# Performance work log

Hardware: AMD Instinct MI355X
Metric: run time of the kernel (lower is better)

Reference implementation:

```python
import jax, jax.numpy as jnp
import numpy as np

EMB = 768
EPS = 1e-5

def setup_inputs() -> dict:
    key = jax.random.key(0)
    ks = jax.random.split(key, 7)
    B, S, D = 8, 2048, EMB
    s = 1.0 / np.sqrt(D)
    return {
        "h_": jax.random.normal(ks[0], (B, S, D), dtype=jnp.float32),
        "ln_gamma": jnp.ones((D,), jnp.float32),
        "ln_beta": jnp.zeros((D,), jnp.float32),
        "wq": jax.random.normal(ks[1], (D, D), jnp.float32) * s,
        "bq": jax.random.normal(ks[2], (D,), jnp.float32) * 0.01,
        "wk": jax.random.normal(ks[3], (D, D), jnp.float32) * s,
        "bk": jax.random.normal(ks[4], (D,), jnp.float32) * 0.01,
    }

def reference(h_, ln_gamma, ln_beta, wq, bq, wk, bk):
    # LayerNorm over last dim
    mu = jnp.mean(h_, axis=-1, keepdims=True)
    var = jnp.mean(jnp.square(h_ - mu), axis=-1, keepdims=True)
    hn = (h_ - mu) * jax.lax.rsqrt(var + EPS) * ln_gamma + ln_beta
    # Q/K projections (torch Linear: x @ W^T + b; here wq is [D_in, D_out])
    q = jnp.einsum('bsd,de->bse', hn, wq) + bq
    k = jnp.einsum('bsd,de->bse', hn, wk) + bk
    # scores: q @ k^T (no sqrt(d) scaling, matching original)
    w = jnp.einsum('bqd,bkd->bqk', q, k)
    return jax.nn.softmax(w, axis=-1)
```

## Files before the change

kernel.cpp:

```cpp
#include <hip/hip_runtime.h>
#include <stdint.h>

#define EMB   768
#define BATCH 8
#define SEQ   2048
#define ROWS  (BATCH*SEQ)
#define EPS   1e-5f

#define BM 128
#define BN 128
#define BK 32
#define BK2 64

typedef _Float16 half8 __attribute__((ext_vector_type(8)));
typedef _Float16 half4 __attribute__((ext_vector_type(4)));
typedef float    floatx4 __attribute__((ext_vector_type(4)));

__device__ __forceinline__ void g2l16(const void* g, void* l) {
    __builtin_amdgcn_global_load_lds(
        (const __attribute__((address_space(1))) unsigned int*)g,
        (__attribute__((address_space(3))) unsigned int*)l,
        16, 0, 0);
}

__global__ __launch_bounds__(256) void split_w_kernel(
    const float* __restrict__ wq, const float* __restrict__ wk,
    _Float16* __restrict__ wq_hi, _Float16* __restrict__ wq_lo,
    _Float16* __restrict__ wk_hi, _Float16* __restrict__ wk_lo)
{
    const float* src = (blockIdx.y == 0) ? wq : wk;
    _Float16* dh     = (blockIdx.y == 0) ? wq_hi : wk_hi;
    _Float16* dl     = (blockIdx.y == 0) ? wq_lo : wk_lo;
    int i4 = blockIdx.x * 256 + threadIdx.x;
    float4 v = ((const float4*)src)[i4];
    half4 vh, vl;
    float c[4] = {v.x, v.y, v.z, v.w};
#pragma unroll
    for (int t = 0; t < 4; t++) {
        _Float16 hi = (_Float16)c[t];
        vh[t] = hi;
        vl[t] = (_Float16)(c[t] - (float)hi);
    }
    ((half4*)dh)[i4] = vh;
    ((half4*)dl)[i4] = vl;
}

__global__ __launch_bounds__(256) void wtilde_kernel(
    const float* __restrict__ wk, const float* __restrict__ bq,
    float* __restrict__ wt)
{
    int row  = blockIdx.x * 4 + (threadIdx.x >> 6);
    int lane = threadIdx.x & 63;
    const float4* r4 = (const float4*)(wk + (size_t)row * EMB);
    const float4* b4 = (const float4*)bq;
    float s = 0.f;
#pragma unroll
    for (int j = 0; j < 3; j++) {
        float4 a = r4[lane + j * 64];
        float4 b = b4[lane + j * 64];
        s += a.x * b.x + a.y * b.y + a.z * b.z + a.w * b.w;
    }
#pragma unroll
    for (int sh = 1; sh < 64; sh <<= 1) s += __shfl_xor(s, sh, 64);
    if (lane == 0) wt[row] = s;
}

__global__ __launch_bounds__(256) void ln_kernel(
    const float* __restrict__ h,
    const float* __restrict__ gamma,
    const float* __restrict__ beta,
    const float* __restrict__ wt,
    _Float16* __restrict__ hn_hi,
    float* __restrict__ v_out)
{
    int row  = blockIdx.x * 4 + (threadIdx.x >> 6);
    int lane = threadIdx.x & 63;
    const float4* hr4 = (const float4*)(h + (size_t)row * EMB);
    float4 x[3];
    float s1 = 0.f, s2 = 0.f;
#pragma unroll
    for (int j = 0; j < 3; j++) {
        x[j] = hr4[lane + j * 64];
        s1 += x[j].x + x[j].y + x[j].z + x[j].w;
        s2 += x[j].x * x[j].x + x[j].y * x[j].y + x[j].z * x[j].z + x[j].w * x[j].w;
    }
#pragma unroll
    for (int s = 1; s < 64; s <<= 1) {
        s1 += __shfl_xor(s1, s, 64);
        s2 += __shfl_xor(s2, s, 64);
    }
    float mu  = s1 * (1.0f / EMB);
    float var = s2 * (1.0f / EMB) - mu * mu;
    float rs  = rsqrtf(var + EPS);
    _Float16* oh = hn_hi + (size_t)row * EMB;
    float vsum = 0.f;
#pragma unroll
    for (int j = 0; j < 3; j++) {
        int e4 = lane + j * 64;
        float4 g = ((const float4*)gamma)[e4];
        float4 b = ((const float4*)beta)[e4];
        float4 w = ((const float4*)wt)[e4];
        float v[4] = {
            (x[j].x - mu) * rs * g.x + b.x,
            (x[j].y - mu) * rs * g.y + b.y,
            (x[j].z - mu) * rs * g.z + b.z,
            (x[j].w - mu) * rs * g.w + b.w };
        vsum += v[0] * w.x + v[1] * w.y + v[2] * w.z + v[3] * w.w;
        half4 vh;
#pragma unroll
        for (int t = 0; t < 4; t++) vh[t] = (_Float16)v[t];
        *(half4*)(oh + e4 * 4) = vh;
    }
#pragma unroll
    for (int s = 1; s < 64; s <<= 1) vsum += __shfl_xor(vsum, s, 64);
    if (lane == 0) v_out[row] = vsum;
}

__global__ __launch_bounds__(256) void gt_kernel(
    const _Float16* __restrict__ wk_hi, const _Float16* __restrict__ wk_lo,
    const _Float16* __restrict__ wq_hi, const _Float16* __restrict__ wq_lo,
    _Float16* __restrict__ gt_hi, _Float16* __restrict__ gt_lo)
{
    __shared__ __attribute__((aligned(16))) _Float16 Ah_s[BM * BK];
    __shared__ __attribute__((aligned(16))) _Float16 Al_s[BM * BK];
    __shared__ __attribute__((aligned(16))) _Float16 Bh_s[BN * BK];
    __shared__ __attribute__((aligned(16))) _Float16 Bl_s[BN * BK];

    int rowbase = blockIdx.y * BM;
    int colbase = blockIdx.x * BN;
    int tid  = threadIdx.x;
    int lane = tid & 63, wave = tid >> 6;
    int wrow = (wave >> 1) * 64, wcol = (wave & 1) * 64;

    floatx4 acc[4][4];
#pragma unroll
    for (int i = 0; i < 4; i++)
#pragma unroll
        for (int j = 0; j < 4; j++) acc[i][j] = (floatx4){0.f, 0.f, 0.f, 0.f};

    size_t arow = (size_t)(rowbase + tid / 4) * EMB;
    size_t brow = (size_t)(colbase + tid / 4) * EMB;
    int    boff = (tid % 4) * 16;
    const char* gAh = (const char*)(wk_hi + arow) + boff;
    const char* gAl = (const char*)(wk_lo + arow) + boff;
    const char* gBh = (const char*)(wq_hi + brow) + boff;
    const char* gBl = (const char*)(wq_lo + brow) + boff;
    char* lAh = (char*)Ah_s + tid * 16;
    char* lAl = (char*)Al_s + tid * 16;
    char* lBh = (char*)Bh_s + tid * 16;
    char* lBl = (char*)Bl_s + tid * 16;
    const size_t half_stride = (size_t)64 * EMB * 2;

    for (int k0 = 0; k0 < EMB; k0 += BK) {
        __syncthreads();
        g2l16(gAh, lAh); g2l16(gAh + half_stride, lAh + 4096);
        g2l16(gAl, lAl); g2l16(gAl + half_stride, lAl + 4096);
        g2l16(gBh, lBh); g2l16(gBh + half_stride, lBh + 4096);
        g2l16(gBl, lBl); g2l16(gBl + half_stride, lBl + 4096);
        gAh += 64; gAl += 64; gBh += 64; gBl += 64;
        __syncthreads();

        half8 ah[4], al[4], bh[4], bl[4];
#pragma unroll
        for (int i = 0; i < 4; i++) {
            int off = (wrow + i * 16 + (lane & 15)) * 64 + (lane >> 4) * 16;
            ah[i] = *(const half8*)((const char*)Ah_s + off);
            al[i] = *(const half8*)((const char*)Al_s + off);
        }
#pragma unroll
        for (int j = 0; j < 4; j++) {
            int off = (wcol + j * 16 + (lane & 15)) * 64 + (lane >> 4) * 16;
            bh[j] = *(const half8*)((const char*)Bh_s + off);
            bl[j] = *(const half8*)((const char*)Bl_s + off);
        }
#pragma unroll
        for (int i = 0; i < 4; i++)
#pragma unroll
            for (int j = 0; j < 4; j++) {
                acc[i][j] = __builtin_amdgcn_mfma_f32_16x16x32_f16(ah[i], bh[j], acc[i][j], 0, 0, 0);
                acc[i][j] = __builtin_amdgcn_mfma_f32_16x16x32_f16(ah[i], bl[j], acc[i][j], 0, 0, 0);
                acc[i][j] = __builtin_amdgcn_mfma_f32_16x16x32_f16(al[i], bh[j], acc[i][j], 0, 0, 0);
            }
    }

#pragma unroll
    for (int j = 0; j < 4; j++) {
        int col = colbase + wcol + j * 16 + (lane & 15);
#pragma unroll
        for (int i = 0; i < 4; i++) {
#pragma unroll
            for (int r = 0; r < 4; r++) {
                int row = rowbase + wrow + i * 16 + (lane >> 4) * 4 + r;
                float v = acc[i][j][r];
                _Float16 hi = (_Float16)v;
                gt_hi[(size_t)row * EMB + col] = hi;
                gt_lo[(size_t)row * EMB + col] = (_Float16)(v - (float)hi);
            }
        }
    }
}

__global__ __launch_bounds__(256) void t_kernel(
    const _Float16* __restrict__ hn_hi,
    const _Float16* __restrict__ gt_hi, const _Float16* __restrict__ gt_lo,
    _Float16* __restrict__ t_hi)
{
    __shared__ __attribute__((aligned(16))) _Float16 Ah_s[BM * BK2];
    __shared__ __attribute__((aligned(16))) _Float16 Bh_s[BN * BK2];
    __shared__ __attribute__((aligned(16))) _Float16 Bl_s[BN * BK2];

    int rowbase = blockIdx.y * BM;
    int colbase = blockIdx.x * BN;
    int tid  = threadIdx.x;
    int lane = tid & 63, wave = tid >> 6;
    int wrow = (wave >> 1) * 64, wcol = (wave & 1) * 64;

    floatx4 acc[4][4];
#pragma unroll
    for (int i = 0; i < 4; i++)
#pragma unroll
        for (int j = 0; j < 4; j++) acc[i][j] = (floatx4){0.f, 0.f, 0.f, 0.f};

    size_t arow = (size_t)(rowbase + tid / 8) * EMB;
    size_t brow = (size_t)(colbase + tid / 8) * EMB;
    int    boff = (tid % 8) * 16;
    const char* gAh = (const char*)(hn_hi + arow) + boff;
    const char* gBh = (const char*)(gt_hi + brow) + boff;
    const char* gBl = (const char*)(gt_lo + brow) + boff;
    char* lAh = (char*)Ah_s + tid * 16;
    char* lBh = (char*)Bh_s + tid * 16;
    char* lBl = (char*)Bl_s + tid * 16;
    const size_t pstride = (size_t)32 * EMB * 2;

    for (int k0 = 0; k0 < EMB; k0 += BK2) {
        __syncthreads();
#pragma unroll
        for (int p = 0; p < 4; p++) {
            g2l16(gAh + p * pstride, lAh + p * 4096);
            g2l16(gBh + p * pstride, lBh + p * 4096);
            g2l16(gBl + p * pstride, lBl + p * 4096);
        }
        gAh += 128; gBh += 128; gBl += 128;
        __syncthreads();

#pragma unroll
        for (int ko = 0; ko < 2; ko++) {
            half8 ah[4], bh[4], bl[4];
#pragma unroll
            for (int i = 0; i < 4; i++) {
                int off = (wrow + i * 16 + (lane & 15)) * 128 + ko * 64 + (lane >> 4) * 16;
                ah[i] = *(const half8*)((const char*)Ah_s + off);
            }
#pragma unroll
            for (int j = 0; j < 4; j++) {
                int off = (wcol + j * 16 + (lane & 15)) * 128 + ko * 64 + (lane >> 4) * 16;
                bh[j] = *(const half8*)((const char*)Bh_s + off);
                bl[j] = *(const half8*)((const char*)Bl_s + off);
            }
#pragma unroll
            for (int i = 0; i < 4; i++)
#pragma unroll
                for (int j = 0; j < 4; j++) {
                    acc[i][j] = __builtin_amdgcn_mfma_f32_16x16x32_f16(ah[i], bh[j], acc[i][j], 0, 0, 0);
                    acc[i][j] = __builtin_amdgcn_mfma_f32_16x16x32_f16(ah[i], bl[j], acc[i][j], 0, 0, 0);
                }
        }
    }

#pragma unroll
    for (int j = 0; j < 4; j++) {
        int col = colbase + wcol + j * 16 + (lane & 15);
#pragma unroll
        for (int i = 0; i < 4; i++) {
#pragma unroll
            for (int r = 0; r < 4; r++) {
                int row = rowbase + wrow + i * 16 + (lane >> 4) * 4 + r;
                t_hi[(size_t)row * EMB + col] = (_Float16)acc[i][j][r];
            }
        }
    }
}

__global__ __launch_bounds__(256) void scores_kernel(
    const _Float16* __restrict__ t_hi,
    const _Float16* __restrict__ hn_hi,
    const float* __restrict__ v_in,
    float* __restrict__ out,
    float2* __restrict__ state)
{
    __shared__ __attribute__((aligned(16))) _Float16 Ah_s[BM * BK2];
    __shared__ __attribute__((aligned(16))) _Float16 Bh_s[BN * BK2];
    __shared__ float red[128][2];

    int b = blockIdx.z;
    size_t base = (size_t)b * SEQ * EMB;
    int rowbase = blockIdx.y * BM;
    int colbase = blockIdx.x * BN;
    int tid  = threadIdx.x;
    int lane = tid & 63, wave = tid >> 6;
    int wrow = (wave >> 1) * 64, wcol = (wave & 1) * 64;

    floatx4 acc[4][4];
#pragma unroll
    for (int i = 0; i < 4; i++)
#pragma unroll
        for (int j = 0; j < 4; j++) acc[i][j] = (floatx4){0.f, 0.f, 0.f, 0.f};

    size_t arow = base + (size_t)(rowbase + tid / 8) * EMB;
    size_t brow = base + (size_t)(colbase + tid / 8) * EMB;
    int    boff = (tid % 8) * 16;
    const char* gAh = (const char*)(t_hi + arow) + boff;
    const char* gBh = (const char*)(hn_hi + brow) + boff;
    char* lAh = (char*)Ah_s + tid * 16;
    char* lBh = (char*)Bh_s + tid * 16;
    const size_t pstride = (size_t)32 * EMB * 2;

    for (int k0 = 0; k0 < EMB; k0 += BK2) {
        __syncthreads();
#pragma unroll
        for (int p = 0; p < 4; p++) {
            g2l16(gAh + p * pstride, lAh + p * 4096);
            g2l16(gBh + p * pstride, lBh + p * 4096);
        }
        gAh += 128; gBh += 128;
        __syncthreads();

#pragma unroll
        for (int ko = 0; ko < 2; ko++) {
            half8 ah[4], bh[4];
#pragma unroll
            for (int i = 0; i < 4; i++) {
                int off = (wrow + i * 16 + (lane & 15)) * 128 + ko * 64 + (lane >> 4) * 16;
                ah[i] = *(const half8*)((const char*)Ah_s + off);
            }
#pragma unroll
            for (int j = 0; j < 4; j++) {
                int off = (wcol + j * 16 + (lane & 15)) * 128 + ko * 64 + (lane >> 4) * 16;
                bh[j] = *(const half8*)((const char*)Bh_s + off);
            }
#pragma unroll
            for (int i = 0; i < 4; i++)
#pragma unroll
                for (int j = 0; j < 4; j++)
                    acc[i][j] = __builtin_amdgcn_mfma_f32_16x16x32_f16(ah[i], bh[j], acc[i][j], 0, 0, 0);
        }
    }

    const float* vb = v_in + (size_t)b * SEQ + colbase;
#pragma unroll
    for (int j = 0; j < 4; j++) {
        float vv = vb[wcol + j * 16 + (lane & 15)];
#pragma unroll
        for (int i = 0; i < 4; i++)
#pragma unroll
            for (int r = 0; r < 4; r++) acc[i][j][r] += vv;
    }

    float m1[4][4];
#pragma unroll
    for (int i = 0; i < 4; i++)
#pragma unroll
        for (int r = 0; r < 4; r++) {
            float m = fmaxf(fmaxf(acc[i][0][r], acc[i][1][r]), fmaxf(acc[i][2][r], acc[i][3][r]));
#pragma unroll
            for (int s = 1; s < 16; s <<= 1) m = fmaxf(m, __shfl_xor(m, s, 64));
            m1[i][r] = m;
        }
    if ((lane & 15) == 0) {
#pragma unroll
        for (int i = 0; i < 4; i++)
#pragma unroll
            for (int r = 0; r < 4; r++)
                red[wrow + i * 16 + (lane >> 4) * 4 + r][wave & 1] = m1[i][r];
    }
    __syncthreads();
    float mrow[4][4];
#pragma unroll
    for (int i = 0; i < 4; i++)
#pragma unroll
        for (int r = 0; r < 4; r++) {
            int rr = wrow + i * 16 + (lane >> 4) * 4 + r;
            mrow[i][r] = fmaxf(red[rr][0], red[rr][1]);
        }
    __syncthreads();

    float ls[4][4];
#pragma unroll
    for (int i = 0; i < 4; i++)
#pragma unroll
        for (int r = 0; r < 4; r++) {
            float s = 0.f;
#pragma unroll
            for (int j = 0; j < 4; j++) {
                float e = __expf(acc[i][j][r] - mrow[i][r]);
                acc[i][j][r] = e;
                s += e;
            }
#pragma unroll
            for (int sh = 1; sh < 16; sh <<= 1) s += __shfl_xor(s, sh, 64);
            ls[i][r] = s;
        }
    if ((lane & 15) == 0) {
#pragma unroll
        for (int i = 0; i < 4; i++)
#pragma unroll
            for (int r = 0; r < 4; r++)
                red[wrow + i * 16 + (lane >> 4) * 4 + r][wave & 1] = ls[i][r];
    }
    __syncthreads();

    size_t outbase = (size_t)b * SEQ * SEQ;
#pragma unroll
    for (int i = 0; i < 4; i++)
#pragma unroll
        for (int j = 0; j < 4; j++)
#pragma unroll
            for (int r = 0; r < 4; r++) {
                int row = rowbase + wrow + i * 16 + (lane >> 4) * 4 + r;
                int col = colbase + wcol + j * 16 + (lane & 15);
                out[outbase + (size_t)row * SEQ + col] = acc[i][j][r];
            }

    if ((wave & 1) == 0 && (lane & 15) == 0) {
#pragma unroll
        for (int i = 0; i < 4; i++)
#pragma unroll
            for (int r = 0; r < 4; r++) {
                int rr = wrow + i * 16 + (lane >> 4) * 4 + r;
                float l = red[rr][0] + red[rr][1];
                state[((size_t)b * SEQ + rowbase + rr) * 16 + blockIdx.x] =
                    make_float2(mrow[i][r], l);
            }
    }
}

__global__ __launch_bounds__(256) void fixup_kernel(
    float* __restrict__ out,
    const float2* __restrict__ state)
{
    int row  = blockIdx.x * 4 + (threadIdx.x >> 6);
    int lane = threadIdx.x & 63;
    const float2* st = state + (size_t)row * 16;
    float m[16], l[16];
    float M = -INFINITY;
#pragma unroll
    for (int t = 0; t < 16; t++) { float2 v = st[t]; m[t] = v.x; l[t] = v.y; M = fmaxf(M, m[t]); }
    float L = 0.f;
#pragma unroll
    for (int t = 0; t < 16; t++) { m[t] = __expf(m[t] - M); L += l[t] * m[t]; }
    float inv = 1.0f / L;
    float4* o4 = (float4*)(out + (size_t)row * SEQ);
#pragma unroll
    for (int c0 = 0; c0 < 8; c0++) {
        int i4 = c0 * 64 + lane;
        float s = m[i4 >> 5] * inv;
        float4 v = o4[i4];
        v.x *= s; v.y *= s; v.z *= s; v.w *= s;
        o4[i4] = v;
    }
}

extern "C" void kernel_launch(void* const* d_in, const int* in_sizes, int n_in,
                              void* d_out, int out_size, void* d_ws, size_t ws_size,
                              hipStream_t stream)
{
    const float* h  = (const float*)d_in[0];
    const float* g  = (const float*)d_in[1];
    const float* be = (const float*)d_in[2];
    const float* wq = (const float*)d_in[3];
    const float* bq = (const float*)d_in[4];
    const float* wk = (const float*)d_in[5];
    const float* bk = (const float*)d_in[6];
    (void)bk;
    float* out = (float*)d_out;

    char* ws = (char*)d_ws;
    const size_t SZ  = (size_t)ROWS * EMB * 2;
    const size_t WSZ = (size_t)EMB * EMB * 2;
    _Float16* hn_hi = (_Float16*)(ws);
    _Float16* t_hi  = (_Float16*)(ws + SZ);
    char* wbase = ws + 2 * SZ;
    _Float16* wq_hi = (_Float16*)(wbase);
    _Float16* wq_lo = (_Float16*)(wbase + WSZ);
    _Float16* wk_hi = (_Float16*)(wbase + 2 * WSZ);
    _Float16* wk_lo = (_Float16*)(wbase + 3 * WSZ);
    _Float16* gt_hi = (_Float16*)(wbase + 4 * WSZ);
    _Float16* gt_lo = (_Float16*)(wbase + 5 * WSZ);
    char* sbase = wbase + 6 * WSZ;
    float*  wt = (float*)(sbase);
    float*  v  = (float*)(sbase + 4096);
    float2* st = (float2*)(sbase + 4096 + 65536);

    split_w_kernel<<<dim3(576, 2), 256, 0, stream>>>(wq, wk, wq_hi, wq_lo, wk_hi, wk_lo);
    wtilde_kernel<<<dim3(EMB / 4), 256, 0, stream>>>(wk, bq, wt);
    ln_kernel<<<dim3(ROWS / 4), 256, 0, stream>>>(h, g, be, wt, hn_hi, v);
    gt_kernel<<<dim3(EMB / BN, EMB / BM), 256, 0, stream>>>(wk_hi, wk_lo, wq_hi, wq_lo, gt_hi, gt_lo);
    t_kernel<<<dim3(EMB / BN, ROWS / BM), 256, 0, stream>>>(hn_hi, gt_hi, gt_lo, t_hi);
    scores_kernel<<<dim3(SEQ / BN, SEQ / BM, BATCH), 256, 0, stream>>>(t_hi, hn_hi, v, out, st);
    fixup_kernel<<<dim3(ROWS / 4), 256, 0, stream>>>(out, st);
}
```

Baseline: 391.9 us.

## Swizzle LDS tiles, stage unnormalized scores in fp16, shuffle-based fixup

Applies XOR swizzles to the LDS tile layouts in the gt, t and scores kernels, meant to remove bank conflicts on the half8 fragment reads. When the workspace is large enough, the scores kernel writes unnormalized exp values as fp16 to a scratch buffer instead of fp32 to the output. The fixup kernel then reads them back and writes normalized fp32. This cuts the bytes of the intermediate write and read, at the cost of fp16 rounding of the partial probabilities. The fixup kernel also reduces the per-tile max and sum state with wave shuffles instead of 16 serial loads per thread.

Measured after the change: 373.5 us. 1.05x faster.

```diff
diff --git a/kernel.cpp b/kernel.cpp
--- a/kernel.cpp
+++ b/kernel.cpp
@@ -140,7 +140,7 @@
 
     size_t arow = (size_t)(rowbase + tid / 4) * EMB;
     size_t brow = (size_t)(colbase + tid / 4) * EMB;
-    int    boff = (tid % 4) * 16;
+    int    boff = (((tid % 4) ^ ((tid >> 3) & 3)) * 16);
     const char* gAh = (const char*)(wk_hi + arow) + boff;
     const char* gAl = (const char*)(wk_lo + arow) + boff;
     const char* gBh = (const char*)(wq_hi + brow) + boff;
@@ -163,13 +163,15 @@
         half8 ah[4], al[4], bh[4], bl[4];
 #pragma unroll
         for (int i = 0; i < 4; i++) {
-            int off = (wrow + i * 16 + (lane & 15)) * 64 + (lane >> 4) * 16;
+            int roff = wrow + i * 16 + (lane & 15);
+            int off = roff * 64 + ((((lane >> 4)) ^ ((roff >> 1) & 3)) * 16);
             ah[i] = *(const half8*)((const char*)Ah_s + off);
             al[i] = *(const half8*)((const char*)Al_s + off);
         }
 #pragma unroll
         for (int j = 0; j < 4; j++) {
-            int off = (wcol + j * 16 + (lane & 15)) * 64 + (lane >> 4) * 16;
+            int coff = wcol + j * 16 + (lane & 15);
+            int off = coff * 64 + ((((lane >> 4)) ^ ((coff >> 1) & 3)) * 16);
             bh[j] = *(const half8*)((const char*)Bh_s + off);
             bl[j] = *(const half8*)((const char*)Bl_s + off);
         }
@@ -223,7 +225,7 @@
 
     size_t arow = (size_t)(rowbase + tid / 8) * EMB;
     size_t brow = (size_t)(colbase + tid / 8) * EMB;
-    int    boff = (tid % 8) * 16;
+    int    boff = (((tid % 8) ^ ((tid >> 3) & 7)) * 16);
     const char* gAh = (const char*)(hn_hi + arow) + boff;
     const char* gBh = (const char*)(gt_hi + brow) + boff;
     const char* gBl = (const char*)(gt_lo + brow) + boff;
@@ -248,12 +250,14 @@
             half8 ah[4], bh[4], bl[4];
 #pragma unroll
             for (int i = 0; i < 4; i++) {
-                int off = (wrow + i * 16 + (lane & 15)) * 128 + ko * 64 + (lane >> 4) * 16;
+                int roff = wrow + i * 16 + (lane & 15);
+                int off = roff * 128 + ((ko * 64 + (lane >> 4) * 16) ^ ((roff & 7) << 4));
                 ah[i] = *(const half8*)((const char*)Ah_s + off);
             }
 #pragma unroll
             for (int j = 0; j < 4; j++) {
-                int off = (wcol + j * 16 + (lane & 15)) * 128 + ko * 64 + (lane >> 4) * 16;
+                int coff = wcol + j * 16 + (lane & 15);
+                int off = coff * 128 + ((ko * 64 + (lane >> 4) * 16) ^ ((coff & 7) << 4));
                 bh[j] = *(const half8*)((const char*)Bh_s + off);
                 bl[j] = *(const half8*)((const char*)Bl_s + off);
             }
@@ -281,11 +285,13 @@
     }
 }
 
+template<bool F16OUT>
 __global__ __launch_bounds__(256) void scores_kernel(
     const _Float16* __restrict__ t_hi,
     const _Float16* __restrict__ hn_hi,
     const float* __restrict__ v_in,
     float* __restrict__ out,
+    _Float16* __restrict__ pt,
     float2* __restrict__ state)
 {
     __shared__ __attribute__((aligned(16))) _Float16 Ah_s[BM * BK2];
@@ -308,7 +314,7 @@
 
     size_t arow = base + (size_t)(rowbase + tid / 8) * EMB;
     size_t brow = base + (size_t)(colbase + tid / 8) * EMB;
-    int    boff = (tid % 8) * 16;
+    int    boff = (((tid % 8) ^ ((tid >> 3) & 7)) * 16);
     const char* gAh = (const char*)(t_hi + arow) + boff;
     const char* gBh = (const char*)(hn_hi + brow) + boff;
     char* lAh = (char*)Ah_s + tid * 16;
@@ -330,12 +336,14 @@
             half8 ah[4], bh[4];
 #pragma unroll
             for (int i = 0; i < 4; i++) {
-                int off = (wrow + i * 16 + (lane & 15)) * 128 + ko * 64 + (lane >> 4) * 16;
+                int roff = wrow + i * 16 + (lane & 15);
+                int off = roff * 128 + ((ko * 64 + (lane >> 4) * 16) ^ ((roff & 7) << 4));
                 ah[i] = *(const half8*)((const char*)Ah_s + off);
             }
 #pragma unroll
             for (int j = 0; j < 4; j++) {
-                int off = (wcol + j * 16 + (lane & 15)) * 128 + ko * 64 + (lane >> 4) * 16;
+                int coff = wcol + j * 16 + (lane & 15);
+                int off = coff * 128 + ((ko * 64 + (lane >> 4) * 16) ^ ((coff & 7) << 4));
                 bh[j] = *(const half8*)((const char*)Bh_s + off);
             }
 #pragma unroll
@@ -418,7 +426,10 @@
             for (int r = 0; r < 4; r++) {
                 int row = rowbase + wrow + i * 16 + (lane >> 4) * 4 + r;
                 int col = colbase + wcol + j * 16 + (lane & 15);
-                out[outbase + (size_t)row * SEQ + col] = acc[i][j][r];
+                if (F16OUT)
+                    pt[outbase + (size_t)row * SEQ + col] = (_Float16)acc[i][j][r];
+                else
+                    out[outbase + (size_t)row * SEQ + col] = acc[i][j][r];
             }
 
     if ((wave & 1) == 0 && (lane & 15) == 0) {
@@ -434,29 +445,50 @@
     }
 }
 
+template<bool F16IN>
 __global__ __launch_bounds__(256) void fixup_kernel(
     float* __restrict__ out,
+    const _Float16* __restrict__ pt,
     const float2* __restrict__ state)
 {
     int row  = blockIdx.x * 4 + (threadIdx.x >> 6);
     int lane = threadIdx.x & 63;
-    const float2* st = state + (size_t)row * 16;
-    float m[16], l[16];
-    float M = -INFINITY;
-#pragma unroll
-    for (int t = 0; t < 16; t++) { float2 v = st[t]; m[t] = v.x; l[t] = v.y; M = fmaxf(M, m[t]); }
-    float L = 0.f;
-#pragma unroll
-    for (int t = 0; t < 16; t++) { m[t] = __expf(m[t] - M); L += l[t] * m[t]; }
-    float inv = 1.0f / L;
-    float4* o4 = (float4*)(out + (size_t)row * SEQ);
-#pragma unroll
-    for (int c0 = 0; c0 < 8; c0++) {
-        int i4 = c0 * 64 + lane;
-        float s = m[i4 >> 5] * inv;
-        float4 v = o4[i4];
-        v.x *= s; v.y *= s; v.z *= s; v.w *= s;
-        o4[i4] = v;
+    float2 v = state[(size_t)row * 16 + (lane & 15)];
+    float M = v.x;
+#pragma unroll
+    for (int s = 1; s < 16; s <<= 1) M = fmaxf(M, __shfl_xor(M, s, 64));
+    float e  = __expf(v.x - M);
+    float Lp = v.y * e;
+#pragma unroll
+    for (int s = 1; s < 16; s <<= 1) Lp += __shfl_xor(Lp, s, 64);
+    float fv = e / Lp;
+
+    if (F16IN) {
+        const half8* p8 = (const half8*)(pt + (size_t)row * SEQ);
+        float4* o4 = (float4*)(out + (size_t)row * SEQ);
+#pragma unroll
+        for (int c0 = 0; c0 < 4; c0++) {
+            int i8 = c0 * 64 + lane;
+            float s = __shfl(fv, i8 >> 4, 64);
+            half8 h = p8[i8];
+            float4 a, bqv;
+            a.x = (float)h[0] * s; a.y = (float)h[1] * s;
+            a.z = (float)h[2] * s; a.w = (float)h[3] * s;
+            bqv.x = (float)h[4] * s; bqv.y = (float)h[5] * s;
+            bqv.z = (float)h[6] * s; bqv.w = (float)h[7] * s;
+            o4[i8 * 2]     = a;
+            o4[i8 * 2 + 1] = bqv;
+        }
+    } else {
+        float4* o4 = (float4*)(out + (size_t)row * SEQ);
+#pragma unroll
+        for (int c0 = 0; c0 < 8; c0++) {
+            int i4 = c0 * 64 + lane;
+            float s = __shfl(fv, i4 >> 5, 64);
+            float4 w = o4[i4];
+            w.x *= s; w.y *= s; w.z *= s; w.w *= s;
+            o4[i4] = w;
+        }
     }
 }
 
@@ -490,12 +522,21 @@
     float*  wt = (float*)(sbase);
     float*  v  = (float*)(sbase + 4096);
     float2* st = (float2*)(sbase + 4096 + 65536);
+    char*   ptb = sbase + 4096 + 65536 + (size_t)ROWS * 16 * sizeof(float2);
+    const size_t PTSZ = (size_t)BATCH * SEQ * SEQ * 2;
+    _Float16* pt = (_Float16*)ptb;
+    bool use_f16 = ws_size >= (size_t)(ptb - ws) + PTSZ;
 
     split_w_kernel<<<dim3(576, 2), 256, 0, stream>>>(wq, wk, wq_hi, wq_lo, wk_hi, wk_lo);
     wtilde_kernel<<<dim3(EMB / 4), 256, 0, stream>>>(wk, bq, wt);
     ln_kernel<<<dim3(ROWS / 4), 256, 0, stream>>>(h, g, be, wt, hn_hi, v);
     gt_kernel<<<dim3(EMB / BN, EMB / BM), 256, 0, stream>>>(wk_hi, wk_lo, wq_hi, wq_lo, gt_hi, gt_lo);
     t_kernel<<<dim3(EMB / BN, ROWS / BM), 256, 0, stream>>>(hn_hi, gt_hi, gt_lo, t_hi);
-    scores_kernel<<<dim3(SEQ / BN, SEQ / BM, BATCH), 256, 0, stream>>>(t_hi, hn_hi, v, out, st);
-    fixup_kernel<<<dim3(ROWS / 4), 256, 0, stream>>>(out, st);
-}
+    if (use_f16) {
+        scores_kernel<true><<<dim3(SEQ / BN, SEQ / BM, BATCH), 256, 0, stream>>>(t_hi, hn_hi, v, out, pt, st);
+        fixup_kernel<true><<<dim3(ROWS / 4), 256, 0, stream>>>(out, pt, st);
+    } else {
+        scores_kernel<false><<<dim3(SEQ / BN, SEQ / BM, BATCH), 256, 0, stream>>>(t_hi, hn_hi, v, out, nullptr, st);
+        fixup_kernel<false><<<dim3(ROWS / 4), 256, 0, stream>>>(out, nullptr, st);
+    }
+}
```
